# Kernel tuning notes

Measured on AMD Instinct MI355X. Metric: run time of the kernel, lower is better.

Reference implementation:

```python
import jax, jax.numpy as jnp
import numpy as np


def setup_inputs() -> dict:
    key = jax.random.key(0)
    k1, k2, k3, k4 = jax.random.split(key, 4)
    B, T, C, H = 8, 2048, 1024, 64
    x = jax.random.normal(k1, (B, T, C), dtype=jnp.float32)
    Wq = jax.random.normal(k2, (C, H), dtype=jnp.float32) * (C ** -0.5)
    Wk = jax.random.normal(k3, (C, H), dtype=jnp.float32) * (C ** -0.5)
    Wv = jax.random.normal(k4, (C, H), dtype=jnp.float32) * (C ** -0.5)
    return {"x": x, "Wq": Wq, "Wk": Wk, "Wv": Wv}


def reference(x, Wq, Wk, Wv):
    # x: [B,T,C]; Wq/Wk/Wv: [C,H] (nn.Linear bias=False => x @ W)
    B, T, C = x.shape
    H = Wq.shape[-1]
    q = jnp.einsum('btc,ch->bth', x, Wq)
    k = jnp.einsum('btc,ch->bth', x, Wk)
    v = jnp.einsum('btc,ch->bth', x, Wv)
    scale = H ** -0.5
    att = jnp.einsum('bqh,bkh->bqk', q, k) * scale  # [B,T,T]
    causal = jnp.tril(jnp.ones((T, T), dtype=bool))
    att = jnp.where(causal, att, -jnp.inf)
    att = jax.nn.softmax(att, axis=-1)
    out = jnp.einsum('bqk,bkh->bqh', att, v)  # [B,T,H]
    return out
```

## Files before the change

### kernel.cpp

```cpp
#include <hip/hip_runtime.h>
#include <hip/hip_bf16.h>
#include <math.h>

#define BB 8
#define TT 2048
#define CC 1024
#define HH 64
#define BT (BB * TT)

typedef __attribute__((ext_vector_type(8))) short short8;
typedef __attribute__((ext_vector_type(4))) float floatx4;

static __device__ inline ushort f2bf(float f) {
    __hip_bfloat16 h = __float2bfloat16(f);
    return *reinterpret_cast<ushort*>(&h);
}
static __device__ inline unsigned int f2bf2(float lo, float hi) {
    __hip_bfloat162 h = __float22bfloat162_rn(make_float2(lo, hi));
    return *reinterpret_cast<unsigned int*>(&h);
}
static __device__ inline float bf2f(ushort u) {
    union { unsigned int i; float f; } c;
    c.i = ((unsigned int)u) << 16;
    return c.f;
}
static __device__ inline void gl_lds16(const ushort* g, ushort* l) {
    __builtin_amdgcn_global_load_lds(
        (const __attribute__((address_space(1))) unsigned int*)g,
        (__attribute__((address_space(3))) unsigned int*)l,
        16, 0, 0);
}

__global__ __launch_bounds__(256) void wprep_kernel(
    const float* __restrict__ Wq, const float* __restrict__ Wk,
    const float* __restrict__ Wv, ushort* __restrict__ WbT)
{
    __shared__ float ws_[64 * 65];
    const int m  = blockIdx.x >> 4;
    const int kb = (blockIdx.x & 15) * 64;
    const float* W = (m == 0) ? Wq : (m == 1) ? Wk : Wv;
    const int t  = threadIdx.x;
    const int lr = t >> 4, lc = (t & 15) * 4;
    #pragma unroll
    for (int i = 0; i < 4; ++i) {
        const int row = lr + i * 16;
        float4 v = *(const float4*)&W[(size_t)(kb + row) * HH + lc];
        ws_[row * 65 + lc + 0] = v.x; ws_[row * 65 + lc + 1] = v.y;
        ws_[row * 65 + lc + 2] = v.z; ws_[row * 65 + lc + 3] = v.w;
    }
    __syncthreads();
    const int n = t & 63, kseg = t >> 6;
    union { ushort s[16]; uint4 q[2]; } u;
    #pragma unroll
    for (int j = 0; j < 16; ++j)
        u.s[j] = f2bf(ws_[(kseg * 16 + j) * 65 + n]);
    ushort* dst = &WbT[(size_t)(m * 64 + n) * 1024 + kb + kseg * 16];
    *(uint4*)&dst[0] = u.q[0];
    *(uint4*)&dst[8] = u.q[1];
}

__global__ __launch_bounds__(256) void qkv_kernel(
    const float* __restrict__ x, const ushort* __restrict__ WbT,
    ushort* __restrict__ qb, ushort* __restrict__ kbS, ushort* __restrict__ vS)
{
    __shared__ ushort As[2][256 * 8];

    const int row0 = blockIdx.x * 32;
    const int t    = threadIdx.x;
    const int w    = t >> 6;
    const int lane = t & 63;
    const int l16  = lane & 15;
    const int quad = lane >> 4;
    const int ct0  = w * 3;

    const int srow = t >> 3, sseg = t & 7;
    const int slot = (((sseg >> 2) * 2 + (srow >> 4)) * 16 + (srow & 15)) * 4 + (sseg & 3);
    const float* xsrc = &x[(size_t)(row0 + srow) * CC + sseg * 8];

    floatx4 acc[2][3];
    #pragma unroll
    for (int mt = 0; mt < 2; ++mt)
        #pragma unroll
        for (int c = 0; c < 3; ++c) acc[mt][c] = (floatx4){0.f, 0.f, 0.f, 0.f};

    float4 xa0 = *(const float4*)&xsrc[0];
    float4 xb0 = *(const float4*)&xsrc[4];
    float4 xa1 = *(const float4*)&xsrc[64];
    float4 xb1 = *(const float4*)&xsrc[68];

    short8 bfr[2][3];
    #pragma unroll
    for (int p = 0; p < 2; ++p)
        #pragma unroll
        for (int c = 0; c < 3; ++c)
            bfr[p][c] = *(const short8*)&WbT[(size_t)((ct0 + c) * 16 + l16) * 1024
                                             + p * 32 + quad * 8];

    auto body = [&](int it, float4& xa, float4& xb) {
        uint4 uq;
        uq.x = f2bf2(xa.x, xa.y); uq.y = f2bf2(xa.z, xa.w);
        uq.z = f2bf2(xb.x, xb.y); uq.w = f2bf2(xb.z, xb.w);
        *(uint4*)&As[it & 1][slot * 8] = uq;
        __syncthreads();

        if (it + 2 < 16) {
            xa = *(const float4*)&xsrc[(it + 2) * 64 + 0];
            xb = *(const float4*)&xsrc[(it + 2) * 64 + 4];
        }
        short8 bnx[2][3];
        if (it < 15) {
            const int kn = (it + 1) * 64;
            #pragma unroll
            for (int p = 0; p < 2; ++p)
                #pragma unroll
                for (int c = 0; c < 3; ++c)
                    bnx[p][c] = *(const short8*)&WbT[(size_t)((ct0 + c) * 16 + l16) * 1024
                                                     + kn + p * 32 + quad * 8];
        }

        #pragma unroll
        for (int p = 0; p < 2; ++p) {
            short8 a0 = *(const short8*)&As[it & 1][(size_t)((p * 2 + 0) * 64 + l16 * 4 + quad) * 8];
            short8 a1 = *(const short8*)&As[it & 1][(size_t)((p * 2 + 1) * 64 + l16 * 4 + quad) * 8];
            #pragma unroll
            for (int c = 0; c < 3; ++c) {
                acc[0][c] = __builtin_amdgcn_mfma_f32_16x16x32_bf16(a0, bfr[p][c], acc[0][c], 0, 0, 0);
                acc[1][c] = __builtin_amdgcn_mfma_f32_16x16x32_bf16(a1, bfr[p][c], acc[1][c], 0, 0, 0);
            }
        }
        #pragma unroll
        for (int p = 0; p < 2; ++p)
            #pragma unroll
            for (int c = 0; c < 3; ++c)
                bfr[p][c] = bnx[p][c];
    };

    for (int it2 = 0; it2 < 16; it2 += 2) {
        body(it2 + 0, xa0, xb0);
        body(it2 + 1, xa1, xb1);
    }

    const int half = (row0 >> 5) & 1;
    const size_t tile = (size_t)(row0 >> 6) * 4096;
    #pragma unroll
    for (int c = 0; c < 3; ++c) {
        const int ct    = ct0 + c;
        const int mtype = ct >> 2;
        const int n0    = (ct & 3) * 16;
        #pragma unroll
        for (int mt = 0; mt < 2; ++mt) {
            const int row = row0 + mt * 16 + quad * 4;
            if (mtype == 0) {
                #pragma unroll
                for (int reg = 0; reg < 4; ++reg)
                    qb[(size_t)(row + reg) * HH + n0 + l16] = f2bf(acc[mt][c][reg] * 0.125f);
            } else if (mtype == 1) {
                const int cP    = half * 2 + mt;
                const int pP    = (ct & 3) >> 1;
                const int quadP = ((ct & 3) * 2 + (l16 >> 3)) & 3;
                const int jP    = l16 & 7;
                const int ub    = (cP * 2 + pP) * 64 + quadP * 16;
                #pragma unroll
                for (int reg = 0; reg < 4; ++reg)
                    kbS[tile + (size_t)(ub + quad * 4 + reg) * 8 + jP] = f2bf(acc[mt][c][reg]);
            } else {
                const int cp2 = (ct & 3) * 2 + half;
                #pragma unroll
                for (int reg = 0; reg < 4; ++reg) {
                    const int rq    = quad * 4 + reg;
                    const int quadP = mt * 2 + (rq >> 3);
                    vS[tile + (size_t)(cp2 * 64 + quadP * 16 + l16) * 8 + (rq & 7)] = f2bf(acc[mt][c][reg]);
                }
            }
        }
    }
}

__global__ __launch_bounds__(256) void attn_kernel(
    const ushort* __restrict__ qb, const ushort* __restrict__ kbS,
    const ushort* __restrict__ vS, ushort* __restrict__ Opart,
    float* __restrict__ ml)
{
    __shared__ __align__(16) ushort Kb[2][4096];
    __shared__ __align__(16) ushort Vb[2][4096];
    __shared__ __align__(16) ushort P[4][16 * 72];

    const int t    = threadIdx.x;
    const int w    = t >> 6;
    const int lane = t & 63;
    const int l16  = lane & 15;
    const int quad = lane >> 4;

    const int b   = blockIdx.x & 7;
    const int idx = blockIdx.x >> 3;
    int qt, part, np;
    if (idx < 32)      { qt = 31 - (idx >> 2); part = idx & 3; np = 4; }
    else if (idx < 56) { const int u = idx - 32; const int g = u / 3;
                         qt = 23 - g; part = u - g * 3; np = 3; }
    else if (idx < 72) { const int u = idx - 56; qt = 15 - (u >> 1); part = u & 1; np = 2; }
    else               { qt = 7 - (idx - 72); part = 0; np = 1; }
    const int ntiles = qt + 1;
    const int ktb = (part * ntiles) / np;
    const int kte = ((part + 1) * ntiles) / np;

    const ushort* ktile0 = kbS + (size_t)(b * 32) * 4096;
    const ushort* vtile0 = vS  + (size_t)(b * 32) * 4096;

    short8 qf[2];
    {
        const ushort* qrow = qb + ((size_t)b * TT + qt * 64 + w * 16) * HH;
        qf[0] = *(const short8*)&qrow[l16 * HH + quad * 8];
        qf[1] = *(const short8*)&qrow[l16 * HH + 32 + quad * 8];
    }
    short8 ones;
    #pragma unroll
    for (int i = 0; i < 8; ++i) ones[i] = (short)0x3F80;

    floatx4 o[4], osum;
    #pragma unroll
    for (int c = 0; c < 4; ++c) o[c] = (floatx4){0.f, 0.f, 0.f, 0.f};
    osum = (floatx4){0.f, 0.f, 0.f, 0.f};

    {
        const ushort* gk = ktile0 + (size_t)ktb * 4096 + w * 1024 + lane * 8;
        const ushort* gv = vtile0 + (size_t)ktb * 4096 + w * 1024 + lane * 8;
        gl_lds16(gk,       &Kb[0][w * 1024]);
        gl_lds16(gk + 512, &Kb[0][w * 1024 + 512]);
        gl_lds16(gv,       &Vb[0][w * 1024]);
        gl_lds16(gv + 512, &Vb[0][w * 1024 + 512]);
    }

    ushort* Pw = &P[w][0];

    for (int kt = ktb; kt < kte; ++kt) {
        const int cur = (kt - ktb) & 1;
        __syncthreads();

        if (kt + 1 < kte) {
            const int nxt = cur ^ 1;
            const ushort* gk = ktile0 + (size_t)(kt + 1) * 4096 + w * 1024 + lane * 8;
            const ushort* gv = vtile0 + (size_t)(kt + 1) * 4096 + w * 1024 + lane * 8;
            gl_lds16(gk,       &Kb[nxt][w * 1024]);
            gl_lds16(gk + 512, &Kb[nxt][w * 1024 + 512]);
            gl_lds16(gv,       &Vb[nxt][w * 1024]);
            gl_lds16(gv + 512, &Vb[nxt][w * 1024 + 512]);
        }

        short8 kf[4][2], vf[4][2];
        #pragma unroll
        for (int c = 0; c < 4; ++c)
            #pragma unroll
            for (int p = 0; p < 2; ++p) {
                kf[c][p] = *(const short8*)&Kb[cur][(size_t)(((c * 2 + p) * 64) + lane) * 8];
                vf[c][p] = *(const short8*)&Vb[cur][(size_t)(((c * 2 + p) * 64) + lane) * 8];
            }

        floatx4 s[4];
        #pragma unroll
        for (int c = 0; c < 4; ++c) s[c] = (floatx4){0.f, 0.f, 0.f, 0.f};
        #pragma unroll
        for (int c = 0; c < 4; ++c)
            #pragma unroll
            for (int p = 0; p < 2; ++p)
                s[c] = __builtin_amdgcn_mfma_f32_16x16x32_bf16(qf[p], kf[c][p], s[c], 0, 0, 0);

        if (kt == ntiles - 1) {
            const int qrow0 = qt * 64 + w * 16 + quad * 4;
            const int key0  = kt * 64;
            #pragma unroll
            for (int c = 0; c < 4; ++c)
                #pragma unroll
                for (int reg = 0; reg < 4; ++reg)
                    if (key0 + c * 16 + l16 > qrow0 + reg) s[c][reg] = -1e30f;
        }

        #pragma unroll
        for (int c = 0; c < 4; ++c)
            #pragma unroll
            for (int reg = 0; reg < 4; ++reg)
                Pw[(quad * 4 + reg) * 72 + c * 16 + l16] = f2bf(__expf(s[c][reg]));

        short8 pf[2];
        pf[0] = *(const short8*)&Pw[l16 * 72 + quad * 8];
        pf[1] = *(const short8*)&Pw[l16 * 72 + 32 + quad * 8];

        #pragma unroll
        for (int p = 0; p < 2; ++p) {
            #pragma unroll
            for (int c = 0; c < 4; ++c)
                o[c] = __builtin_amdgcn_mfma_f32_16x16x32_bf16(pf[p], vf[c][p], o[c], 0, 0, 0);
            osum = __builtin_amdgcn_mfma_f32_16x16x32_bf16(pf[p], ones, osum, 0, 0, 0);
        }
    }

    const size_t ub = (size_t)blockIdx.x * 4096;
    #pragma unroll
    for (int c = 0; c < 4; ++c)
        #pragma unroll
        for (int reg = 0; reg < 4; ++reg)
            Opart[ub + (w * 16 + quad * 4 + reg) * 64 + c * 16 + l16] = f2bf(o[c][reg]);
    if (l16 == 0) {
        #pragma unroll
        for (int reg = 0; reg < 4; ++reg)
            ml[(size_t)blockIdx.x * 64 + w * 16 + quad * 4 + reg] = osum[reg];
    }
}

__global__ __launch_bounds__(256) void merge_kernel(
    const ushort* __restrict__ Opart, const float* __restrict__ ml,
    float* __restrict__ out)
{
    const int t    = threadIdx.x;
    const int gw   = blockIdx.x * 4 + (t >> 6);
    const int lane = t & 63;
    const int b    = gw >> 8;
    const int v    = gw & 255;
    const int qt   = v >> 3;
    const int oct  = v & 7;

    int base, np;
    if (qt >= 24)      { base = (31 - qt) * 4;      np = 4; }
    else if (qt >= 16) { base = 32 + (23 - qt) * 3; np = 3; }
    else if (qt >= 8)  { base = 56 + (15 - qt) * 2; np = 2; }
    else               { base = 72 + (7 - qt);      np = 1; }

    const int r4 = lane >> 4;
    const int cs = (lane & 15) * 4;
    float* obase = out + ((size_t)b * TT + qt * 64) * HH;

    #pragma unroll
    for (int rg = 0; rg < 2; ++rg) {
        const int row = oct * 8 + rg * 4 + r4;
        float den = 0.f;
        float ax = 0.f, ay = 0.f, az = 0.f, aw = 0.f;
        for (int p = 0; p < np; ++p) {
            const int unit = (base + p) * 8 + b;
            den += ml[(size_t)unit * 64 + row];
            ushort4 ov = *(const ushort4*)&Opart[(size_t)unit * 4096 + row * 64 + cs];
            ax += bf2f(ov.x); ay += bf2f(ov.y); az += bf2f(ov.z); aw += bf2f(ov.w);
        }
        const float inv = 1.0f / den;
        float4 o4;
        o4.x = ax * inv; o4.y = ay * inv; o4.z = az * inv; o4.w = aw * inv;
        *(float4*)&obase[(size_t)row * HH + cs] = o4;
    }
}

extern "C" void kernel_launch(void* const* d_in, const int* in_sizes, int n_in,
                              void* d_out, int out_size, void* d_ws, size_t ws_size,
                              hipStream_t stream)
{
    (void)in_sizes; (void)n_in; (void)out_size; (void)ws_size;
    const float* x  = (const float*)d_in[0];
    const float* Wq = (const float*)d_in[1];
    const float* Wk = (const float*)d_in[2];
    const float* Wv = (const float*)d_in[3];
    float* outp = (float*)d_out;

    char* base = (char*)d_ws;
    ushort* WbT   = (ushort*)(base);
    ushort* qbuf  = (ushort*)(base + 393216);
    ushort* kbS   = qbuf + (size_t)BT * HH;
    ushort* vSb   = kbS + (size_t)BT * HH;
    ushort* Opart = vSb + (size_t)BT * HH;
    float*  ml    = (float*)((char*)Opart + (size_t)640 * 4096 * 2);

    wprep_kernel<<<dim3(48),  256, 0, stream>>>(Wq, Wk, Wv, WbT);
    qkv_kernel  <<<dim3(512), 256, 0, stream>>>(x, WbT, qbuf, kbS, vSb);
    attn_kernel <<<dim3(640), 256, 0, stream>>>(qbuf, kbS, vSb, Opart, ml);
    merge_kernel<<<dim3(512), 256, 0, stream>>>(Opart, ml, outp);
}
```

Before: 140.4 us.

## Load K/V fragments directly from global, transpose S MFMA, vectorize P stores

Drops the LDS double-buffered K/V staging and its per-tile __syncthreads. Each wave now reads its MFMA fragments straight from global memory, relying on L2/L1 reuse across the four waves. The QK^T MFMA operands are swapped so each lane holds a contiguous row of scores, which allows packed bf16x2 8-byte stores of P into LDS instead of scalar stores. s_setprio wraps the MFMA sections. The trade-off is redundant global/L2 traffic per wave and exposed load latency with no prefetch, in exchange for removing barriers and LDS pressure.

```diff
diff --git a/kernel.cpp b/kernel.cpp
--- a/kernel.cpp
+++ b/kernel.cpp
@@ -23,12 +23,6 @@
     union { unsigned int i; float f; } c;
     c.i = ((unsigned int)u) << 16;
     return c.f;
-}
-static __device__ inline void gl_lds16(const ushort* g, ushort* l) {
-    __builtin_amdgcn_global_load_lds(
-        (const __attribute__((address_space(1))) unsigned int*)g,
-        (__attribute__((address_space(3))) unsigned int*)l,
-        16, 0, 0);
 }
 
 __global__ __launch_bounds__(256) void wprep_kernel(
@@ -181,8 +175,6 @@
     const ushort* __restrict__ vS, ushort* __restrict__ Opart,
     float* __restrict__ ml)
 {
-    __shared__ __align__(16) ushort Kb[2][4096];
-    __shared__ __align__(16) ushort Vb[2][4096];
     __shared__ __align__(16) ushort P[4][16 * 72];
 
     const int t    = threadIdx.x;
@@ -221,69 +213,55 @@
     for (int c = 0; c < 4; ++c) o[c] = (floatx4){0.f, 0.f, 0.f, 0.f};
     osum = (floatx4){0.f, 0.f, 0.f, 0.f};
 
-    {
-        const ushort* gk = ktile0 + (size_t)ktb * 4096 + w * 1024 + lane * 8;
-        const ushort* gv = vtile0 + (size_t)ktb * 4096 + w * 1024 + lane * 8;
-        gl_lds16(gk,       &Kb[0][w * 1024]);
-        gl_lds16(gk + 512, &Kb[0][w * 1024 + 512]);
-        gl_lds16(gv,       &Vb[0][w * 1024]);
-        gl_lds16(gv + 512, &Vb[0][w * 1024 + 512]);
-    }
-
     ushort* Pw = &P[w][0];
 
     for (int kt = ktb; kt < kte; ++kt) {
-        const int cur = (kt - ktb) & 1;
-        __syncthreads();
-
-        if (kt + 1 < kte) {
-            const int nxt = cur ^ 1;
-            const ushort* gk = ktile0 + (size_t)(kt + 1) * 4096 + w * 1024 + lane * 8;
-            const ushort* gv = vtile0 + (size_t)(kt + 1) * 4096 + w * 1024 + lane * 8;
-            gl_lds16(gk,       &Kb[nxt][w * 1024]);
-            gl_lds16(gk + 512, &Kb[nxt][w * 1024 + 512]);
-            gl_lds16(gv,       &Vb[nxt][w * 1024]);
-            gl_lds16(gv + 512, &Vb[nxt][w * 1024 + 512]);
-        }
+        const ushort* kg = ktile0 + (size_t)kt * 4096;
+        const ushort* vg = vtile0 + (size_t)kt * 4096;
 
         short8 kf[4][2], vf[4][2];
         #pragma unroll
         for (int c = 0; c < 4; ++c)
             #pragma unroll
             for (int p = 0; p < 2; ++p) {
-                kf[c][p] = *(const short8*)&Kb[cur][(size_t)(((c * 2 + p) * 64) + lane) * 8];
-                vf[c][p] = *(const short8*)&Vb[cur][(size_t)(((c * 2 + p) * 64) + lane) * 8];
+                kf[c][p] = *(const short8*)&kg[(size_t)(((c * 2 + p) * 64) + lane) * 8];
+                vf[c][p] = *(const short8*)&vg[(size_t)(((c * 2 + p) * 64) + lane) * 8];
             }
 
         floatx4 s[4];
         #pragma unroll
         for (int c = 0; c < 4; ++c) s[c] = (floatx4){0.f, 0.f, 0.f, 0.f};
+        __builtin_amdgcn_s_setprio(1);
         #pragma unroll
         for (int c = 0; c < 4; ++c)
             #pragma unroll
             for (int p = 0; p < 2; ++p)
-                s[c] = __builtin_amdgcn_mfma_f32_16x16x32_bf16(qf[p], kf[c][p], s[c], 0, 0, 0);
+                s[c] = __builtin_amdgcn_mfma_f32_16x16x32_bf16(kf[c][p], qf[p], s[c], 0, 0, 0);
+        __builtin_amdgcn_s_setprio(0);
 
         if (kt == ntiles - 1) {
-            const int qrow0 = qt * 64 + w * 16 + quad * 4;
-            const int key0  = kt * 64;
+            const int key0 = kt * 64 + quad * 4;
+            const int qrow = qt * 64 + w * 16 + l16;
             #pragma unroll
             for (int c = 0; c < 4; ++c)
                 #pragma unroll
                 for (int reg = 0; reg < 4; ++reg)
-                    if (key0 + c * 16 + l16 > qrow0 + reg) s[c][reg] = -1e30f;
-        }
-
-        #pragma unroll
-        for (int c = 0; c < 4; ++c)
-            #pragma unroll
-            for (int reg = 0; reg < 4; ++reg)
-                Pw[(quad * 4 + reg) * 72 + c * 16 + l16] = f2bf(__expf(s[c][reg]));
+                    if (key0 + c * 16 + reg > qrow) s[c][reg] = -1e30f;
+        }
+
+        #pragma unroll
+        for (int c = 0; c < 4; ++c) {
+            uint2 u;
+            u.x = f2bf2(__expf(s[c][0]), __expf(s[c][1]));
+            u.y = f2bf2(__expf(s[c][2]), __expf(s[c][3]));
+            *(uint2*)&Pw[l16 * 72 + c * 16 + quad * 4] = u;
+        }
 
         short8 pf[2];
         pf[0] = *(const short8*)&Pw[l16 * 72 + quad * 8];
         pf[1] = *(const short8*)&Pw[l16 * 72 + 32 + quad * 8];
 
+        __builtin_amdgcn_s_setprio(1);
         #pragma unroll
         for (int p = 0; p < 2; ++p) {
             #pragma unroll
@@ -291,6 +269,7 @@
                 o[c] = __builtin_amdgcn_mfma_f32_16x16x32_bf16(pf[p], vf[c][p], o[c], 0, 0, 0);
             osum = __builtin_amdgcn_mfma_f32_16x16x32_bf16(pf[p], ones, osum, 0, 0, 0);
         }
+        __builtin_amdgcn_s_setprio(0);
     }
 
     const size_t ub = (size_t)blockIdx.x * 4096;
```

Result: no change. 140.0 us (-0.3%).
